# Optimization experiments

Hardware: AMD Instinct MI355X
Metric: run time of the kernel (lower is better)

## Reference

```python
import jax, jax.numpy as jnp
from jax import lax
import numpy as np

ALPHA = 0.82
MAXITER = 10
N1_NODES = 2048
N2_NODES = 2048
K_ATTR = 64
EDGE_P = 0.004  # sparse-ish adjacency density


def setup_inputs() -> dict:
    key = jax.random.key(0)
    k1, k2, k3, k4 = jax.random.split(key, 4)
    A1 = (jax.random.uniform(k1, (N1_NODES, N1_NODES)) < EDGE_P).astype(jnp.float32)
    A1 = jnp.maximum(A1, A1.T)  # undirected 0/1 adjacency
    A2 = (jax.random.uniform(k2, (N2_NODES, N2_NODES)) < EDGE_P).astype(jnp.float32)
    A2 = jnp.maximum(A2, A2.T)
    N1 = jax.random.uniform(k3, (N1_NODES, K_ATTR), dtype=jnp.float32)
    N2 = jax.random.uniform(k4, (N2_NODES, K_ATTR), dtype=jnp.float32)
    # default prior (_get_H with path=None), normalized so sum ~= 1
    H = jnp.full((N2_NODES, N1_NODES), 1.0 / (N1_NODES * N2_NODES), dtype=jnp.float32)
    return {"A1": A1, "A2": A2, "N1": N1, "N2": N2, "H": H}


def _row_l2_normalize(N):
    nrm = jnp.sqrt(jnp.sum(N * N, axis=1, keepdims=True))
    return jnp.where(nrm > 0, N / jnp.where(nrm > 0, nrm, 1.0), 0.0)


def _final_forward(A1, A2, N1, N2, H, alpha=ALPHA, maxiter=MAXITER):
    # No edge attrs: L=1, E1=A1, E2=A2. T = 1/A^2 where A^2>0 (elementwise),
    # E <- E*T, so B = (E*A) = A*T*A.
    def masked_recip_sq(A):
        A2e = A * A
        return jnp.where(A2e > 0, 1.0 / jnp.where(A2e > 0, A2e, 1.0), 0.0)

    B1 = (A1 * masked_recip_sq(A1)) * A1  # (n1, n1)
    B2 = (A2 * masked_recip_sq(A2)) * A2  # (n2, n2)

    N1n = _row_l2_normalize(N1)  # (n1, K)
    N2n = _row_l2_normalize(N2)  # (n2, K)

    # Kronecker vectors laid out as (n1, n2) matrices (C-order == kron order):
    # N[i*n2+j] = sum_k N1[i,k]*N2[j,k]  -> N1n @ N2n.T
    Nm = N1n @ N2n.T  # (n1, n2)
    dm = (B1 @ N1n) @ (B2 @ N2n).T  # (n1, n2)
    D = Nm * dm
    DD = jnp.where(D > 0, lax.rsqrt(jnp.where(D > 0, D, 1.0)), 0.0)  # inf -> 0
    q = DD * Nm  # (n1, n2)

    # h = H.flatten('F') with H (n2,n1): as an (n1,n2) matrix this is H.T
    h = H.T  # (n1, n2)

    def step(s, _):
        # M = (q*s) reshaped (n2,n1) F-order == (q*s).T in our layout.
        # S = B2 @ M @ B1 (n2,n1); S.flatten('F') as (n1,n2) == B1.T @ (q*s) @ B2.T
        S_t = B1.T @ (q * s) @ B2.T  # (n1, n2)
        s_new = (1.0 - alpha) * h + alpha * q * S_t
        return s_new, None

    s, _ = lax.scan(step, h, None, length=maxiter)
    # original: s.reshape((n1, n2)) C-order -> exactly our layout
    return s  # (n1, n2) alignment matrix


def reference(A1, A2, N1, N2, H):
    return _final_forward(A1, A2, N1, N2, H)
```

## Files before the change

### kernel.cpp

```cpp
#include <hip/hip_runtime.h>

#define NMAT 2048
#define KATTR 64
#define CAP 128
#define NITER 10

typedef unsigned short ushort4v __attribute__((ext_vector_type(4)));

__device__ __forceinline__ unsigned short f2bf(float f) {
  unsigned u = __float_as_uint(f);
  return (unsigned short)((u + 0x7fff + ((u >> 16) & 1)) >> 16);
}
__device__ __forceinline__ float bf2f(unsigned short b) {
  return __uint_as_float((unsigned)b << 16);
}
__device__ __forceinline__ float bflo(unsigned v) {
  return __uint_as_float(v << 16);
}
__device__ __forceinline__ float bfhi(unsigned v) {
  return __uint_as_float(v & 0xffff0000u);
}
__device__ __forceinline__ int swz(int c) { return 4 * c + (((c >> 3) & 7) << 2); }

__global__ __launch_bounds__(256) void k_build(
    const float* __restrict__ A, unsigned short* __restrict__ idx,
    unsigned short* __restrict__ idxT, int* __restrict__ cnt) {
  __shared__ int lcnt;
  int r = blockIdx.x;
  if (threadIdx.x == 0) lcnt = 0;
  __syncthreads();
  const float* row = A + (size_t)r * NMAT;
  for (int c = threadIdx.x; c < NMAT; c += 256) {
    if (row[c] != 0.0f) {
      int p = atomicAdd(&lcnt, 1);
      if (p < CAP) {
        idx[r * CAP + p] = (unsigned short)c;
        if (idxT) idxT[(size_t)p * NMAT + r] = (unsigned short)c;
      }
    }
  }
  __syncthreads();
  if (threadIdx.x == 0) cnt[r] = lcnt < CAP ? lcnt : CAP;
}

__global__ __launch_bounds__(256) void k_norm(const float* __restrict__ Nin,
                                              float* __restrict__ Nout) {
  int row = blockIdx.x * 4 + (threadIdx.x >> 6);
  int lane = threadIdx.x & 63;
  float v = Nin[(size_t)row * KATTR + lane];
  float ss = v * v;
#pragma unroll
  for (int o = 32; o > 0; o >>= 1) ss += __shfl_xor(ss, o);
  float nrm = sqrtf(ss);
  Nout[(size_t)row * KATTR + lane] = (nrm > 0.f) ? v / nrm : 0.f;
}

__global__ void k_gatherN(const unsigned short* __restrict__ idx,
                          const int* __restrict__ cnt,
                          const float* __restrict__ Nn,
                          float* __restrict__ C) {
  int i = blockIdx.x;
  int lane = threadIdx.x;
  int nn = cnt[i];
  const unsigned short* ip = idx + i * CAP;
  float acc = 0.f;
  for (int t = 0; t < nn; ++t) {
    int k = ip[t];
    acc += Nn[(size_t)k * KATTR + lane];
  }
  C[(size_t)i * KATTR + lane] = acc;
}

__global__ __launch_bounds__(256) void k_transpose(const float* __restrict__ H,
                                                   float* __restrict__ Ht) {
  __shared__ float tile[64][65];
  int j0 = blockIdx.x * 64;
  int i0 = blockIdx.y * 64;
  int c = threadIdx.x & 63;
  int r0 = threadIdx.x >> 6;
  for (int r = r0; r < 64; r += 4)
    tile[r][c] = H[(size_t)(j0 + r) * NMAT + i0 + c];
  __syncthreads();
  for (int r = r0; r < 64; r += 4)
    Ht[(size_t)(i0 + r) * NMAT + j0 + c] = tile[c][r];
}

__global__ __launch_bounds__(256) void k_q(
    const float* __restrict__ N1n, const float* __restrict__ C1,
    const float* __restrict__ N2n, const float* __restrict__ C2,
    const float* __restrict__ Ht, float* __restrict__ q,
    float* __restrict__ Q2, unsigned short* __restrict__ M,
    unsigned short* __restrict__ M0base) {
  __shared__ float sA[64][68];
  __shared__ float sB[64][68];
  int i0 = blockIdx.y * 64, j0 = blockIdx.x * 64;
  int c = threadIdx.x & 63, r0 = threadIdx.x >> 6;
  int tx = threadIdx.x & 15, ty = threadIdx.x >> 4;
  const float alpha = 0.82f;

  float nmv[4][4] = {};
  float dmv[4][4] = {};

  for (int r = r0; r < 64; r += 4) {
    sA[c][r] = N1n[(size_t)(i0 + r) * KATTR + c];
    sB[c][r] = N2n[(size_t)(j0 + r) * KATTR + c];
  }
  __syncthreads();
#pragma unroll 4
  for (int k = 0; k < 64; ++k) {
    float4 a = *(const float4*)&sA[k][ty * 4];
    float4 b = *(const float4*)&sB[k][tx * 4];
    float av[4] = {a.x, a.y, a.z, a.w};
    float bv[4] = {b.x, b.y, b.z, b.w};
#pragma unroll
    for (int ii = 0; ii < 4; ++ii)
#pragma unroll
      for (int jj = 0; jj < 4; ++jj)
        nmv[ii][jj] = fmaf(av[ii], bv[jj], nmv[ii][jj]);
  }
  __syncthreads();
  for (int r = r0; r < 64; r += 4) {
    sA[c][r] = C1[(size_t)(i0 + r) * KATTR + c];
    sB[c][r] = C2[(size_t)(j0 + r) * KATTR + c];
  }
  __syncthreads();
#pragma unroll 4
  for (int k = 0; k < 64; ++k) {
    float4 a = *(const float4*)&sA[k][ty * 4];
    float4 b = *(const float4*)&sB[k][tx * 4];
    float av[4] = {a.x, a.y, a.z, a.w};
    float bv[4] = {b.x, b.y, b.z, b.w};
#pragma unroll
    for (int ii = 0; ii < 4; ++ii)
#pragma unroll
      for (int jj = 0; jj < 4; ++jj)
        dmv[ii][jj] = fmaf(av[ii], bv[jj], dmv[ii][jj]);
  }

#pragma unroll
  for (int ii = 0; ii < 4; ++ii) {
    int i = i0 + ty * 4 + ii;
    size_t base = (size_t)i * NMAT + j0 + tx * 4;
    float4 hv = *(const float4*)&Ht[base];
    float hvv[4] = {hv.x, hv.y, hv.z, hv.w};
    float qv[4], q2v[4];
    ushort4v mv, m0v;
#pragma unroll
    for (int jj = 0; jj < 4; ++jj) {
      float nmx = nmv[ii][jj];
      float D = nmx * dmv[ii][jj];
      float qq = (D > 0.f) ? nmx * rsqrtf(D) : 0.f;
      qv[jj] = qq;
      q2v[jj] = alpha * qq * qq;
      float m0 = qq * hvv[jj];
      mv[jj] = f2bf(m0);
      m0v[jj] = f2bf((1.0f - alpha) * m0);
    }
    *(float4*)&q[base] = make_float4(qv[0], qv[1], qv[2], qv[3]);
    *(float4*)&Q2[base] = make_float4(q2v[0], q2v[1], q2v[2], q2v[3]);
    *(ushort4v*)&M[base] = mv;
    *(ushort4v*)&M0base[base] = m0v;
  }
}

__global__ __launch_bounds__(1024, 8) void k_iter(
    const unsigned short* __restrict__ idx1, const int* __restrict__ cnt1,
    const unsigned short* __restrict__ idx2T, const int* __restrict__ cnt2,
    const unsigned short* __restrict__ Min, const float* __restrict__ MinF,
    const float* __restrict__ Q2, const unsigned short* __restrict__ M0base,
    const float* __restrict__ q, const float* __restrict__ Ht,
    unsigned short* __restrict__ Mout, float* __restrict__ MoutF,
    float* __restrict__ sout, int in32, int out32, int last) {
  __shared__ float lds[4 * NMAT + 32];
  int i0 = blockIdx.x * 4;
  int tid = threadIdx.x;
  int c0 = tid * 2;

  float acc[4][2];
#pragma unroll
  for (int r = 0; r < 4; ++r) {
    int nn = cnt1[i0 + r];
    const unsigned short* ip = idx1 + (i0 + r) * CAP;
    float a0 = 0.f, a1 = 0.f;
    float b0 = 0.f, b1 = 0.f;
    if (in32) {
      int t = 0;
      for (; t + 4 <= nn; t += 4) {
        uint2 pk = *(const uint2*)(ip + t);
        int k0 = pk.x & 0xffff, k1 = pk.x >> 16;
        int k2 = pk.y & 0xffff, k3 = pk.y >> 16;
        float2 v0 = *(const float2*)(MinF + (size_t)k0 * NMAT + c0);
        float2 v1 = *(const float2*)(MinF + (size_t)k1 * NMAT + c0);
        float2 v2 = *(const float2*)(MinF + (size_t)k2 * NMAT + c0);
        float2 v3 = *(const float2*)(MinF + (size_t)k3 * NMAT + c0);
        a0 += v0.x + v1.x; a1 += v0.y + v1.y;
        b0 += v2.x + v3.x; b1 += v2.y + v3.y;
      }
      for (; t < nn; ++t) {
        float2 v0 = *(const float2*)(MinF + (size_t)ip[t] * NMAT + c0);
        a0 += v0.x; a1 += v0.y;
      }
    } else {
      int t = 0;
      for (; t + 8 <= nn; t += 8) {
        uint4 pk = *(const uint4*)(ip + t);
        int k0 = pk.x & 0xffff, k1 = pk.x >> 16;
        int k2 = pk.y & 0xffff, k3 = pk.y >> 16;
        int k4 = pk.z & 0xffff, k5 = pk.z >> 16;
        int k6 = pk.w & 0xffff, k7 = pk.w >> 16;
        unsigned v0 = *(const unsigned*)(Min + (size_t)k0 * NMAT + c0);
        unsigned v1 = *(const unsigned*)(Min + (size_t)k1 * NMAT + c0);
        unsigned v2 = *(const unsigned*)(Min + (size_t)k2 * NMAT + c0);
        unsigned v3 = *(const unsigned*)(Min + (size_t)k3 * NMAT + c0);
        unsigned v4 = *(const unsigned*)(Min + (size_t)k4 * NMAT + c0);
        unsigned v5 = *(const unsigned*)(Min + (size_t)k5 * NMAT + c0);
        unsigned v6 = *(const unsigned*)(Min + (size_t)k6 * NMAT + c0);
        unsigned v7 = *(const unsigned*)(Min + (size_t)k7 * NMAT + c0);
        a0 += bflo(v0) + bflo(v1) + bflo(v2) + bflo(v3);
        a1 += bfhi(v0) + bfhi(v1) + bfhi(v2) + bfhi(v3);
        b0 += bflo(v4) + bflo(v5) + bflo(v6) + bflo(v7);
        b1 += bfhi(v4) + bfhi(v5) + bfhi(v6) + bfhi(v7);
      }
      for (; t + 4 <= nn; t += 4) {
        uint2 pk = *(const uint2*)(ip + t);
        int k0 = pk.x & 0xffff, k1 = pk.x >> 16;
        int k2 = pk.y & 0xffff, k3 = pk.y >> 16;
        unsigned v0 = *(const unsigned*)(Min + (size_t)k0 * NMAT + c0);
        unsigned v1 = *(const unsigned*)(Min + (size_t)k1 * NMAT + c0);
        unsigned v2 = *(const unsigned*)(Min + (size_t)k2 * NMAT + c0);
        unsigned v3 = *(const unsigned*)(Min + (size_t)k3 * NMAT + c0);
        a0 += bflo(v0) + bflo(v1) + bflo(v2) + bflo(v3);
        a1 += bfhi(v0) + bfhi(v1) + bfhi(v2) + bfhi(v3);
      }
      for (; t < nn; ++t) {
        unsigned v0 = *(const unsigned*)(Min + (size_t)ip[t] * NMAT + c0);
        a0 += bflo(v0); a1 += bfhi(v0);
      }
    }
    acc[r][0] = a0 + b0;
    acc[r][1] = a1 + b1;
  }
  *(float4*)&lds[swz(c0)] =
      make_float4(acc[0][0], acc[1][0], acc[2][0], acc[3][0]);
  *(float4*)&lds[swz(c0 + 1)] =
      make_float4(acc[0][1], acc[1][1], acc[2][1], acc[3][1]);
  __syncthreads();

  const float alpha = 0.82f;
  const float oma = 1.0f - alpha;
#pragma unroll
  for (int jj = 0; jj < 2; ++jj) {
    int j = jj * 1024 + tid;
    int nn = cnt2[j];
    const unsigned short* ip = idx2T + j;
    float s0 = 0.f, s1 = 0.f, s2 = 0.f, s3 = 0.f;
    float u0 = 0.f, u1 = 0.f, u2 = 0.f, u3 = 0.f;
    int t = 0;
    for (; t + 4 <= nn; t += 4) {
      int ka = ip[(size_t)t * NMAT];
      int kb = ip[(size_t)(t + 1) * NMAT];
      int kc = ip[(size_t)(t + 2) * NMAT];
      int kd = ip[(size_t)(t + 3) * NMAT];
      float4 va = *(const float4*)&lds[swz(ka)];
      float4 vb = *(const float4*)&lds[swz(kb)];
      float4 vc = *(const float4*)&lds[swz(kc)];
      float4 vd = *(const float4*)&lds[swz(kd)];
      s0 += va.x + vc.x; s1 += va.y + vc.y;
      s2 += va.z + vc.z; s3 += va.w + vc.w;
      u0 += vb.x + vd.x; u1 += vb.y + vd.y;
      u2 += vb.z + vd.z; u3 += vb.w + vd.w;
    }
    for (; t < nn; ++t) {
      int ka = ip[(size_t)t * NMAT];
      float4 va = *(const float4*)&lds[swz(ka)];
      s0 += va.x; s1 += va.y; s2 += va.z; s3 += va.w;
    }
    float sa[4] = {s0 + u0, s1 + u1, s2 + u2, s3 + u3};
    if (last) {
#pragma unroll
      for (int r = 0; r < 4; ++r) {
        size_t off = (size_t)(i0 + r) * NMAT + j;
        sout[off] = oma * Ht[off] + alpha * q[off] * sa[r];
      }
    } else if (out32) {
#pragma unroll
      for (int r = 0; r < 4; ++r) {
        size_t off = (size_t)(i0 + r) * NMAT + j;
        MoutF[off] = fmaf(Q2[off], sa[r], bf2f(M0base[off]));
      }
    } else {
#pragma unroll
      for (int r = 0; r < 4; ++r) {
        size_t off = (size_t)(i0 + r) * NMAT + j;
        Mout[off] = f2bf(fmaf(Q2[off], sa[r], bf2f(M0base[off])));
      }
    }
  }
}

extern "C" void kernel_launch(void* const* d_in, const int* in_sizes, int n_in,
                              void* d_out, int out_size, void* d_ws,
                              size_t ws_size, hipStream_t stream) {
  const float* A1 = (const float*)d_in[0];
  const float* A2 = (const float*)d_in[1];
  const float* N1 = (const float*)d_in[2];
  const float* N2 = (const float*)d_in[3];
  const float* H = (const float*)d_in[4];
  float* s_out = (float*)d_out;

  char* p = (char*)d_ws;
  auto take = [&](size_t bytes) {
    char* r = p;
    p += (bytes + 255) & ~(size_t)255;
    return r;
  };
  unsigned short* idx1 = (unsigned short*)take((size_t)NMAT * CAP * 2);
  unsigned short* idx2 = (unsigned short*)take((size_t)NMAT * CAP * 2);
  unsigned short* idx2T = (unsigned short*)take((size_t)CAP * NMAT * 2);
  int* cnt1 = (int*)take((size_t)NMAT * 4);
  int* cnt2 = (int*)take((size_t)NMAT * 4);
  float* N1n = (float*)take((size_t)NMAT * KATTR * 4);
  float* N2n = (float*)take((size_t)NMAT * KATTR * 4);
  float* C1 = (float*)take((size_t)NMAT * KATTR * 4);
  float* C2 = (float*)take((size_t)NMAT * KATTR * 4);
  float* Ht = (float*)take((size_t)NMAT * NMAT * 4);
  float* q = (float*)take((size_t)NMAT * NMAT * 4);
  float* Q2 = (float*)take((size_t)NMAT * NMAT * 4);
  unsigned short* Mb0 = (unsigned short*)take((size_t)NMAT * NMAT * 2);
  unsigned short* Mb1 = (unsigned short*)take((size_t)NMAT * NMAT * 2);
  unsigned short* M0b = (unsigned short*)take((size_t)NMAT * NMAT * 2);
  float* Mf = (float*)take((size_t)NMAT * NMAT * 4);
  if ((size_t)(p - (char*)d_ws) > ws_size) return;

  k_build<<<NMAT, 256, 0, stream>>>(A1, idx1, (unsigned short*)nullptr, cnt1);
  k_build<<<NMAT, 256, 0, stream>>>(A2, idx2, idx2T, cnt2);
  k_norm<<<NMAT / 4, 256, 0, stream>>>(N1, N1n);
  k_norm<<<NMAT / 4, 256, 0, stream>>>(N2, N2n);
  k_gatherN<<<NMAT, 64, 0, stream>>>(idx1, cnt1, N1n, C1);
  k_gatherN<<<NMAT, 64, 0, stream>>>(idx2, cnt2, N2n, C2);
  k_transpose<<<dim3(32, 32), 256, 0, stream>>>(H, Ht);
  k_q<<<dim3(32, 32), 256, 0, stream>>>(N1n, C1, N2n, C2, Ht, q, Q2, Mb0,
                                        M0b);
  for (int it = 0; it < NITER; ++it) {
    const unsigned short* Min = (it & 1) ? Mb1 : Mb0;
    unsigned short* Mout = (it & 1) ? Mb0 : Mb1;
    int in32 = (it == NITER - 1) ? 1 : 0;
    int out32 = (it == NITER - 2) ? 1 : 0;
    int last = (it == NITER - 1) ? 1 : 0;
    k_iter<<<NMAT / 4, 1024, 0, stream>>>(idx1, cnt1, idx2T, cnt2, Min, Mf,
                                          Q2, M0b, q, Ht, Mout, Mf, s_out,
                                          in32, out32, last);
  }
}
```

Measured before the change: 460.3 us.

## Restructure sparse iteration kernel: 2 rows per block, wide loads, bf16 LDS, grouped indices

The k_iter kernel now handles 2 output rows per block with 256 threads, each loading 8 contiguous columns per gathered row as 16-byte vectors instead of 4-byte loads. The intermediate row products are stored in LDS as packed bf16 pairs (or float2 on the last step), and the transposed index array is regrouped in blocks of 4 so the second gather fetches 4 indices per load. Epilogue operands are prefetched before the reduction loop. This targets memory-transaction count and index-load overhead, but it adds bf16 rounding of the intermediate in LDS and gives each block fewer rows to reuse the gathered index lists across.

```diff
diff --git a/kernel.cpp b/kernel.cpp
--- a/kernel.cpp
+++ b/kernel.cpp
@@ -20,11 +20,21 @@
 __device__ __forceinline__ float bfhi(unsigned v) {
   return __uint_as_float(v & 0xffff0000u);
 }
-__device__ __forceinline__ int swz(int c) { return 4 * c + (((c >> 3) & 7) << 2); }
+
+__device__ __forceinline__ void addv8(float* a, uint4 v) {
+  a[0] += bflo(v.x); a[1] += bfhi(v.x);
+  a[2] += bflo(v.y); a[3] += bfhi(v.y);
+  a[4] += bflo(v.z); a[5] += bfhi(v.z);
+  a[6] += bflo(v.w); a[7] += bfhi(v.w);
+}
+__device__ __forceinline__ void addf8(float* a, float4 x, float4 y) {
+  a[0] += x.x; a[1] += x.y; a[2] += x.z; a[3] += x.w;
+  a[4] += y.x; a[5] += y.y; a[6] += y.z; a[7] += y.w;
+}
 
 __global__ __launch_bounds__(256) void k_build(
     const float* __restrict__ A, unsigned short* __restrict__ idx,
-    unsigned short* __restrict__ idxT, int* __restrict__ cnt) {
+    unsigned short* __restrict__ idxT4, int* __restrict__ cnt) {
   __shared__ int lcnt;
   int r = blockIdx.x;
   if (threadIdx.x == 0) lcnt = 0;
@@ -35,7 +45,9 @@
       int p = atomicAdd(&lcnt, 1);
       if (p < CAP) {
         idx[r * CAP + p] = (unsigned short)c;
-        if (idxT) idxT[(size_t)p * NMAT + r] = (unsigned short)c;
+        if (idxT4)
+          idxT4[(size_t)(p >> 2) * (NMAT * 4) + r * 4 + (p & 3)] =
+              (unsigned short)c;
       }
     }
   }
@@ -163,137 +175,166 @@
   }
 }
 
-__global__ __launch_bounds__(1024, 8) void k_iter(
+__global__ __launch_bounds__(256, 4) void k_iter(
     const unsigned short* __restrict__ idx1, const int* __restrict__ cnt1,
-    const unsigned short* __restrict__ idx2T, const int* __restrict__ cnt2,
+    const unsigned short* __restrict__ idx2T4, const int* __restrict__ cnt2,
     const unsigned short* __restrict__ Min, const float* __restrict__ MinF,
     const float* __restrict__ Q2, const unsigned short* __restrict__ M0base,
     const float* __restrict__ q, const float* __restrict__ Ht,
     unsigned short* __restrict__ Mout, float* __restrict__ MoutF,
     float* __restrict__ sout, int in32, int out32, int last) {
-  __shared__ float lds[4 * NMAT + 32];
-  int i0 = blockIdx.x * 4;
+  __shared__ float2 ldsF[NMAT + 8];
+  unsigned* ldsU = (unsigned*)ldsF;
+  const int GS = NMAT * 4;
+  int i0 = blockIdx.x * 2;
   int tid = threadIdx.x;
-  int c0 = tid * 2;
-
-  float acc[4][2];
-#pragma unroll
-  for (int r = 0; r < 4; ++r) {
+  int c0 = tid * 8;
+
+  float acc[2][8] = {};
+#pragma unroll
+  for (int r = 0; r < 2; ++r) {
     int nn = cnt1[i0 + r];
     const unsigned short* ip = idx1 + (i0 + r) * CAP;
-    float a0 = 0.f, a1 = 0.f;
-    float b0 = 0.f, b1 = 0.f;
+    float* a = acc[r];
+    int t = 0;
     if (in32) {
-      int t = 0;
+      const float* Mb = MinF;
       for (; t + 4 <= nn; t += 4) {
         uint2 pk = *(const uint2*)(ip + t);
         int k0 = pk.x & 0xffff, k1 = pk.x >> 16;
         int k2 = pk.y & 0xffff, k3 = pk.y >> 16;
-        float2 v0 = *(const float2*)(MinF + (size_t)k0 * NMAT + c0);
-        float2 v1 = *(const float2*)(MinF + (size_t)k1 * NMAT + c0);
-        float2 v2 = *(const float2*)(MinF + (size_t)k2 * NMAT + c0);
-        float2 v3 = *(const float2*)(MinF + (size_t)k3 * NMAT + c0);
-        a0 += v0.x + v1.x; a1 += v0.y + v1.y;
-        b0 += v2.x + v3.x; b1 += v2.y + v3.y;
+        const float* p0 = Mb + (size_t)k0 * NMAT + c0;
+        const float* p1 = Mb + (size_t)k1 * NMAT + c0;
+        const float* p2 = Mb + (size_t)k2 * NMAT + c0;
+        const float* p3 = Mb + (size_t)k3 * NMAT + c0;
+        float4 x0 = *(const float4*)p0, y0 = *(const float4*)(p0 + 4);
+        float4 x1 = *(const float4*)p1, y1 = *(const float4*)(p1 + 4);
+        float4 x2 = *(const float4*)p2, y2 = *(const float4*)(p2 + 4);
+        float4 x3 = *(const float4*)p3, y3 = *(const float4*)(p3 + 4);
+        addf8(a, x0, y0); addf8(a, x1, y1);
+        addf8(a, x2, y2); addf8(a, x3, y3);
       }
       for (; t < nn; ++t) {
-        float2 v0 = *(const float2*)(MinF + (size_t)ip[t] * NMAT + c0);
-        a0 += v0.x; a1 += v0.y;
+        const float* p0 = Mb + (size_t)ip[t] * NMAT + c0;
+        addf8(a, *(const float4*)p0, *(const float4*)(p0 + 4));
       }
     } else {
-      int t = 0;
       for (; t + 8 <= nn; t += 8) {
         uint4 pk = *(const uint4*)(ip + t);
         int k0 = pk.x & 0xffff, k1 = pk.x >> 16;
         int k2 = pk.y & 0xffff, k3 = pk.y >> 16;
         int k4 = pk.z & 0xffff, k5 = pk.z >> 16;
         int k6 = pk.w & 0xffff, k7 = pk.w >> 16;
-        unsigned v0 = *(const unsigned*)(Min + (size_t)k0 * NMAT + c0);
-        unsigned v1 = *(const unsigned*)(Min + (size_t)k1 * NMAT + c0);
-        unsigned v2 = *(const unsigned*)(Min + (size_t)k2 * NMAT + c0);
-        unsigned v3 = *(const unsigned*)(Min + (size_t)k3 * NMAT + c0);
-        unsigned v4 = *(const unsigned*)(Min + (size_t)k4 * NMAT + c0);
-        unsigned v5 = *(const unsigned*)(Min + (size_t)k5 * NMAT + c0);
-        unsigned v6 = *(const unsigned*)(Min + (size_t)k6 * NMAT + c0);
-        unsigned v7 = *(const unsigned*)(Min + (size_t)k7 * NMAT + c0);
-        a0 += bflo(v0) + bflo(v1) + bflo(v2) + bflo(v3);
-        a1 += bfhi(v0) + bfhi(v1) + bfhi(v2) + bfhi(v3);
-        b0 += bflo(v4) + bflo(v5) + bflo(v6) + bflo(v7);
-        b1 += bfhi(v4) + bfhi(v5) + bfhi(v6) + bfhi(v7);
+        uint4 v0 = *(const uint4*)(Min + (size_t)k0 * NMAT + c0);
+        uint4 v1 = *(const uint4*)(Min + (size_t)k1 * NMAT + c0);
+        uint4 v2 = *(const uint4*)(Min + (size_t)k2 * NMAT + c0);
+        uint4 v3 = *(const uint4*)(Min + (size_t)k3 * NMAT + c0);
+        uint4 v4 = *(const uint4*)(Min + (size_t)k4 * NMAT + c0);
+        uint4 v5 = *(const uint4*)(Min + (size_t)k5 * NMAT + c0);
+        uint4 v6 = *(const uint4*)(Min + (size_t)k6 * NMAT + c0);
+        uint4 v7 = *(const uint4*)(Min + (size_t)k7 * NMAT + c0);
+        addv8(a, v0); addv8(a, v1); addv8(a, v2); addv8(a, v3);
+        addv8(a, v4); addv8(a, v5); addv8(a, v6); addv8(a, v7);
       }
       for (; t + 4 <= nn; t += 4) {
         uint2 pk = *(const uint2*)(ip + t);
         int k0 = pk.x & 0xffff, k1 = pk.x >> 16;
         int k2 = pk.y & 0xffff, k3 = pk.y >> 16;
-        unsigned v0 = *(const unsigned*)(Min + (size_t)k0 * NMAT + c0);
-        unsigned v1 = *(const unsigned*)(Min + (size_t)k1 * NMAT + c0);
-        unsigned v2 = *(const unsigned*)(Min + (size_t)k2 * NMAT + c0);
-        unsigned v3 = *(const unsigned*)(Min + (size_t)k3 * NMAT + c0);
-        a0 += bflo(v0) + bflo(v1) + bflo(v2) + bflo(v3);
-        a1 += bfhi(v0) + bfhi(v1) + bfhi(v2) + bfhi(v3);
+        uint4 v0 = *(const uint4*)(Min + (size_t)k0 * NMAT + c0);
+        uint4 v1 = *(const uint4*)(Min + (size_t)k1 * NMAT + c0);
+        uint4 v2 = *(const uint4*)(Min + (size_t)k2 * NMAT + c0);
+        uint4 v3 = *(const uint4*)(Min + (size_t)k3 * NMAT + c0);
+        addv8(a, v0); addv8(a, v1); addv8(a, v2); addv8(a, v3);
       }
       for (; t < nn; ++t) {
-        unsigned v0 = *(const unsigned*)(Min + (size_t)ip[t] * NMAT + c0);
-        a0 += bflo(v0); a1 += bfhi(v0);
-      }
-    }
-    acc[r][0] = a0 + b0;
-    acc[r][1] = a1 + b1;
-  }
-  *(float4*)&lds[swz(c0)] =
-      make_float4(acc[0][0], acc[1][0], acc[2][0], acc[3][0]);
-  *(float4*)&lds[swz(c0 + 1)] =
-      make_float4(acc[0][1], acc[1][1], acc[2][1], acc[3][1]);
+        addv8(a, *(const uint4*)(Min + (size_t)ip[t] * NMAT + c0));
+      }
+    }
+  }
+  if (in32) {
+#pragma unroll
+    for (int cc = 0; cc < 8; ++cc)
+      ldsF[c0 + cc] = make_float2(acc[0][cc], acc[1][cc]);
+  } else {
+    unsigned u[8];
+#pragma unroll
+    for (int cc = 0; cc < 8; ++cc)
+      u[cc] = (unsigned)f2bf(acc[0][cc]) | ((unsigned)f2bf(acc[1][cc]) << 16);
+    *(uint4*)&ldsU[c0] = make_uint4(u[0], u[1], u[2], u[3]);
+    *(uint4*)&ldsU[c0 + 4] = make_uint4(u[4], u[5], u[6], u[7]);
+  }
   __syncthreads();
 
   const float alpha = 0.82f;
   const float oma = 1.0f - alpha;
 #pragma unroll
-  for (int jj = 0; jj < 2; ++jj) {
-    int j = jj * 1024 + tid;
+  for (int jj = 0; jj < 8; ++jj) {
+    int j = jj * 256 + tid;
     int nn = cnt2[j];
-    const unsigned short* ip = idx2T + j;
-    float s0 = 0.f, s1 = 0.f, s2 = 0.f, s3 = 0.f;
-    float u0 = 0.f, u1 = 0.f, u2 = 0.f, u3 = 0.f;
+    const unsigned short* bp = idx2T4 + j * 4;
+    size_t off0 = (size_t)i0 * NMAT + j;
+    size_t off1 = off0 + NMAT;
+    float e0a, e0b, e1a, e1b;
+    if (last) {
+      e0a = Ht[off0]; e0b = q[off0];
+      e1a = Ht[off1]; e1b = q[off1];
+    } else {
+      e0a = Q2[off0]; e0b = bf2f(M0base[off0]);
+      e1a = Q2[off1]; e1b = bf2f(M0base[off1]);
+    }
+    float s0 = 0.f, s1 = 0.f;
     int t = 0;
-    for (; t + 4 <= nn; t += 4) {
-      int ka = ip[(size_t)t * NMAT];
-      int kb = ip[(size_t)(t + 1) * NMAT];
-      int kc = ip[(size_t)(t + 2) * NMAT];
-      int kd = ip[(size_t)(t + 3) * NMAT];
-      float4 va = *(const float4*)&lds[swz(ka)];
-      float4 vb = *(const float4*)&lds[swz(kb)];
-      float4 vc = *(const float4*)&lds[swz(kc)];
-      float4 vd = *(const float4*)&lds[swz(kd)];
-      s0 += va.x + vc.x; s1 += va.y + vc.y;
-      s2 += va.z + vc.z; s3 += va.w + vc.w;
-      u0 += vb.x + vd.x; u1 += vb.y + vd.y;
-      u2 += vb.z + vd.z; u3 += vb.w + vd.w;
-    }
-    for (; t < nn; ++t) {
-      int ka = ip[(size_t)t * NMAT];
-      float4 va = *(const float4*)&lds[swz(ka)];
-      s0 += va.x; s1 += va.y; s2 += va.z; s3 += va.w;
-    }
-    float sa[4] = {s0 + u0, s1 + u1, s2 + u2, s3 + u3};
+    if (in32) {
+      for (; t + 4 <= nn; t += 4) {
+        uint2 ga = *(const uint2*)(bp + (size_t)(t >> 2) * GS);
+        float2 va = ldsF[ga.x & 0xffff];
+        float2 vb = ldsF[ga.x >> 16];
+        float2 vc = ldsF[ga.y & 0xffff];
+        float2 vd = ldsF[ga.y >> 16];
+        s0 += (va.x + vb.x) + (vc.x + vd.x);
+        s1 += (va.y + vb.y) + (vc.y + vd.y);
+      }
+      for (; t < nn; ++t) {
+        int k = bp[(size_t)(t >> 2) * GS + (t & 3)];
+        float2 v = ldsF[k];
+        s0 += v.x; s1 += v.y;
+      }
+    } else {
+      for (; t + 8 <= nn; t += 8) {
+        const unsigned short* gp = bp + (size_t)(t >> 2) * GS;
+        uint2 ga = *(const uint2*)gp;
+        uint2 gb = *(const uint2*)(gp + GS);
+        unsigned w0 = ldsU[ga.x & 0xffff], w1 = ldsU[ga.x >> 16];
+        unsigned w2 = ldsU[ga.y & 0xffff], w3 = ldsU[ga.y >> 16];
+        unsigned w4 = ldsU[gb.x & 0xffff], w5 = ldsU[gb.x >> 16];
+        unsigned w6 = ldsU[gb.y & 0xffff], w7 = ldsU[gb.y >> 16];
+        s0 += (bflo(w0) + bflo(w1)) + (bflo(w2) + bflo(w3)) +
+              (bflo(w4) + bflo(w5)) + (bflo(w6) + bflo(w7));
+        s1 += (bfhi(w0) + bfhi(w1)) + (bfhi(w2) + bfhi(w3)) +
+              (bfhi(w4) + bfhi(w5)) + (bfhi(w6) + bfhi(w7));
+      }
+      for (; t + 4 <= nn; t += 4) {
+        uint2 ga = *(const uint2*)(bp + (size_t)(t >> 2) * GS);
+        unsigned w0 = ldsU[ga.x & 0xffff], w1 = ldsU[ga.x >> 16];
+        unsigned w2 = ldsU[ga.y & 0xffff], w3 = ldsU[ga.y >> 16];
+        s0 += (bflo(w0) + bflo(w1)) + (bflo(w2) + bflo(w3));
+        s1 += (bfhi(w0) + bfhi(w1)) + (bfhi(w2) + bfhi(w3));
+      }
+      for (; t < nn; ++t) {
+        int k = bp[(size_t)(t >> 2) * GS + (t & 3)];
+        unsigned w = ldsU[k];
+        s0 += bflo(w); s1 += bfhi(w);
+      }
+    }
     if (last) {
-#pragma unroll
-      for (int r = 0; r < 4; ++r) {
-        size_t off = (size_t)(i0 + r) * NMAT + j;
-        sout[off] = oma * Ht[off] + alpha * q[off] * sa[r];
-      }
+      sout[off0] = oma * e0a + alpha * e0b * s0;
+      sout[off1] = oma * e1a + alpha * e1b * s1;
     } else if (out32) {
-#pragma unroll
-      for (int r = 0; r < 4; ++r) {
-        size_t off = (size_t)(i0 + r) * NMAT + j;
-        MoutF[off] = fmaf(Q2[off], sa[r], bf2f(M0base[off]));
-      }
+      MoutF[off0] = fmaf(e0a, s0, e0b);
+      MoutF[off1] = fmaf(e1a, s1, e1b);
     } else {
-#pragma unroll
-      for (int r = 0; r < 4; ++r) {
-        size_t off = (size_t)(i0 + r) * NMAT + j;
-        Mout[off] = f2bf(fmaf(Q2[off], sa[r], bf2f(M0base[off])));
-      }
+      Mout[off0] = f2bf(fmaf(e0a, s0, e0b));
+      Mout[off1] = f2bf(fmaf(e1a, s1, e1b));
     }
   }
 }
@@ -316,7 +357,7 @@
   };
   unsigned short* idx1 = (unsigned short*)take((size_t)NMAT * CAP * 2);
   unsigned short* idx2 = (unsigned short*)take((size_t)NMAT * CAP * 2);
-  unsigned short* idx2T = (unsigned short*)take((size_t)CAP * NMAT * 2);
+  unsigned short* idx2T4 = (unsigned short*)take((size_t)CAP * NMAT * 2);
   int* cnt1 = (int*)take((size_t)NMAT * 4);
   int* cnt2 = (int*)take((size_t)NMAT * 4);
   float* N1n = (float*)take((size_t)NMAT * KATTR * 4);
@@ -333,7 +374,7 @@
   if ((size_t)(p - (char*)d_ws) > ws_size) return;
 
   k_build<<<NMAT, 256, 0, stream>>>(A1, idx1, (unsigned short*)nullptr, cnt1);
-  k_build<<<NMAT, 256, 0, stream>>>(A2, idx2, idx2T, cnt2);
+  k_build<<<NMAT, 256, 0, stream>>>(A2, idx2, idx2T4, cnt2);
   k_norm<<<NMAT / 4, 256, 0, stream>>>(N1, N1n);
   k_norm<<<NMAT / 4, 256, 0, stream>>>(N2, N2n);
   k_gatherN<<<NMAT, 64, 0, stream>>>(idx1, cnt1, N1n, C1);
@@ -347,8 +388,8 @@
     int in32 = (it == NITER - 1) ? 1 : 0;
     int out32 = (it == NITER - 2) ? 1 : 0;
     int last = (it == NITER - 1) ? 1 : 0;
-    k_iter<<<NMAT / 4, 1024, 0, stream>>>(idx1, cnt1, idx2T, cnt2, Min, Mf,
-                                          Q2, M0b, q, Ht, Mout, Mf, s_out,
-                                          in32, out32, last);
-  }
-}
+    k_iter<<<NMAT / 2, 256, 0, stream>>>(idx1, cnt1, idx2T4, cnt2, Min, Mf,
+                                         Q2, M0b, q, Ht, Mout, Mf, s_out,
+                                         in32, out32, last);
+  }
+}
```

Result: slower. 554.5 us (+20.5%).

## Pad sparse index lists with sentinels and pack coefficients into one bf16 word

Applied to the files above, without the earlier changes.

Pads each adjacency row's neighbour list with sentinel indices that point at a zero row (in global memory) or a zero LDS slot. The gather loops can then issue a fixed unrolled batch of 16–32 loads with no count-dependent tails, and remainder loops only run for high-degree rows. The transposed index array is re-laid-out in groups of 4 so each thread fetches 4 indices per uint2 load. Q2 and M0base are packed as two bf16 halves of one 32-bit word and loaded before the gather, which cuts per-iteration traffic. The cost is wasted loads on low-degree rows and Q2 dropping from fp32 to bf16 precision.

```diff
diff --git a/kernel.cpp b/kernel.cpp
--- a/kernel.cpp
+++ b/kernel.cpp
@@ -4,6 +4,8 @@
 #define KATTR 64
 #define CAP 128
 #define NITER 10
+#define SENT_A 2048
+#define SENT_B 2057
 
 typedef unsigned short ushort4v __attribute__((ext_vector_type(4)));
 
@@ -24,7 +26,7 @@
 
 __global__ __launch_bounds__(256) void k_build(
     const float* __restrict__ A, unsigned short* __restrict__ idx,
-    unsigned short* __restrict__ idxT, int* __restrict__ cnt) {
+    unsigned short* __restrict__ idxT4, int* __restrict__ cnt) {
   __shared__ int lcnt;
   int r = blockIdx.x;
   if (threadIdx.x == 0) lcnt = 0;
@@ -35,12 +37,21 @@
       int p = atomicAdd(&lcnt, 1);
       if (p < CAP) {
         idx[r * CAP + p] = (unsigned short)c;
-        if (idxT) idxT[(size_t)p * NMAT + r] = (unsigned short)c;
-      }
-    }
-  }
-  __syncthreads();
-  if (threadIdx.x == 0) cnt[r] = lcnt < CAP ? lcnt : CAP;
+        if (idxT4)
+          idxT4[(size_t)(p >> 2) * (NMAT * 4) + r * 4 + (p & 3)] =
+              (unsigned short)c;
+      }
+    }
+  }
+  __syncthreads();
+  int n = lcnt < CAP ? lcnt : CAP;
+  for (int p = n + threadIdx.x; p < CAP; p += 256) {
+    idx[r * CAP + p] = (unsigned short)SENT_A;
+    if (idxT4)
+      idxT4[(size_t)(p >> 2) * (NMAT * 4) + r * 4 + (p & 3)] =
+          (unsigned short)SENT_B;
+  }
+  if (threadIdx.x == 0) cnt[r] = n;
 }
 
 __global__ __launch_bounds__(256) void k_norm(const float* __restrict__ Nin,
@@ -85,12 +96,22 @@
     Ht[(size_t)(i0 + r) * NMAT + j0 + c] = tile[c][r];
 }
 
+__global__ __launch_bounds__(1024) void k_zrow(unsigned short* __restrict__ Mb0,
+                                               unsigned short* __restrict__ Mb1,
+                                               float* __restrict__ Mf) {
+  size_t Z = (size_t)NMAT * NMAT;
+  for (int o = threadIdx.x; o < NMAT; o += 1024) {
+    Mb0[Z + o] = 0;
+    Mb1[Z + o] = 0;
+    Mf[Z + o] = 0.f;
+  }
+}
+
 __global__ __launch_bounds__(256) void k_q(
     const float* __restrict__ N1n, const float* __restrict__ C1,
     const float* __restrict__ N2n, const float* __restrict__ C2,
     const float* __restrict__ Ht, float* __restrict__ q,
-    float* __restrict__ Q2, unsigned short* __restrict__ M,
-    unsigned short* __restrict__ M0base) {
+    unsigned* __restrict__ QM, unsigned short* __restrict__ M) {
   __shared__ float sA[64][68];
   __shared__ float sB[64][68];
   int i0 = blockIdx.y * 64, j0 = blockIdx.x * 64;
@@ -143,102 +164,138 @@
     size_t base = (size_t)i * NMAT + j0 + tx * 4;
     float4 hv = *(const float4*)&Ht[base];
     float hvv[4] = {hv.x, hv.y, hv.z, hv.w};
-    float qv[4], q2v[4];
-    ushort4v mv, m0v;
+    float qv[4];
+    unsigned qmv[4];
+    ushort4v mv;
 #pragma unroll
     for (int jj = 0; jj < 4; ++jj) {
       float nmx = nmv[ii][jj];
       float D = nmx * dmv[ii][jj];
       float qq = (D > 0.f) ? nmx * rsqrtf(D) : 0.f;
       qv[jj] = qq;
-      q2v[jj] = alpha * qq * qq;
       float m0 = qq * hvv[jj];
       mv[jj] = f2bf(m0);
-      m0v[jj] = f2bf((1.0f - alpha) * m0);
+      qmv[jj] = (unsigned)f2bf(alpha * qq * qq) |
+                ((unsigned)f2bf((1.0f - alpha) * m0) << 16);
     }
     *(float4*)&q[base] = make_float4(qv[0], qv[1], qv[2], qv[3]);
-    *(float4*)&Q2[base] = make_float4(q2v[0], q2v[1], q2v[2], q2v[3]);
+    *(uint4*)&QM[base] = make_uint4(qmv[0], qmv[1], qmv[2], qmv[3]);
     *(ushort4v*)&M[base] = mv;
-    *(ushort4v*)&M0base[base] = m0v;
   }
 }
 
 __global__ __launch_bounds__(1024, 8) void k_iter(
     const unsigned short* __restrict__ idx1, const int* __restrict__ cnt1,
-    const unsigned short* __restrict__ idx2T, const int* __restrict__ cnt2,
+    const unsigned short* __restrict__ idx2T4, const int* __restrict__ cnt2,
     const unsigned short* __restrict__ Min, const float* __restrict__ MinF,
-    const float* __restrict__ Q2, const unsigned short* __restrict__ M0base,
-    const float* __restrict__ q, const float* __restrict__ Ht,
-    unsigned short* __restrict__ Mout, float* __restrict__ MoutF,
-    float* __restrict__ sout, int in32, int out32, int last) {
-  __shared__ float lds[4 * NMAT + 32];
+    const unsigned* __restrict__ QM, const float* __restrict__ q,
+    const float* __restrict__ Ht, unsigned short* __restrict__ Mout,
+    float* __restrict__ MoutF, float* __restrict__ sout, int in32, int out32,
+    int last) {
+  __shared__ float lds[4 * NMAT + 64];
+  const int GS = NMAT * 4;
   int i0 = blockIdx.x * 4;
   int tid = threadIdx.x;
   int c0 = tid * 2;
 
+  if (tid == 0) *(float4*)&lds[swz(SENT_B)] = make_float4(0.f, 0.f, 0.f, 0.f);
+
   float acc[4][2];
 #pragma unroll
   for (int r = 0; r < 4; ++r) {
     int nn = cnt1[i0 + r];
     const unsigned short* ip = idx1 + (i0 + r) * CAP;
+    uint4 pA = *(const uint4*)(ip);
+    uint4 pB = *(const uint4*)(ip + 8);
+    uint4 pC = *(const uint4*)(ip + 16);
+    uint4 pD = *(const uint4*)(ip + 24);
     float a0 = 0.f, a1 = 0.f;
-    float b0 = 0.f, b1 = 0.f;
     if (in32) {
-      int t = 0;
-      for (; t + 4 <= nn; t += 4) {
-        uint2 pk = *(const uint2*)(ip + t);
-        int k0 = pk.x & 0xffff, k1 = pk.x >> 16;
-        int k2 = pk.y & 0xffff, k3 = pk.y >> 16;
-        float2 v0 = *(const float2*)(MinF + (size_t)k0 * NMAT + c0);
-        float2 v1 = *(const float2*)(MinF + (size_t)k1 * NMAT + c0);
-        float2 v2 = *(const float2*)(MinF + (size_t)k2 * NMAT + c0);
-        float2 v3 = *(const float2*)(MinF + (size_t)k3 * NMAT + c0);
-        a0 += v0.x + v1.x; a1 += v0.y + v1.y;
-        b0 += v2.x + v3.x; b1 += v2.y + v3.y;
-      }
-      for (; t < nn; ++t) {
-        float2 v0 = *(const float2*)(MinF + (size_t)ip[t] * NMAT + c0);
-        a0 += v0.x; a1 += v0.y;
+      const float* Bf = MinF + c0;
+      auto g8f = [&](uint4 pk, float2* w) {
+        w[0] = *(const float2*)(Bf + (size_t)(pk.x & 0xffff) * NMAT);
+        w[1] = *(const float2*)(Bf + (size_t)(pk.x >> 16) * NMAT);
+        w[2] = *(const float2*)(Bf + (size_t)(pk.y & 0xffff) * NMAT);
+        w[3] = *(const float2*)(Bf + (size_t)(pk.y >> 16) * NMAT);
+        w[4] = *(const float2*)(Bf + (size_t)(pk.z & 0xffff) * NMAT);
+        w[5] = *(const float2*)(Bf + (size_t)(pk.z >> 16) * NMAT);
+        w[6] = *(const float2*)(Bf + (size_t)(pk.w & 0xffff) * NMAT);
+        w[7] = *(const float2*)(Bf + (size_t)(pk.w >> 16) * NMAT);
+      };
+      float2 w[16];
+      g8f(pA, w);
+      g8f(pB, w + 8);
+#pragma unroll
+      for (int e = 0; e < 16; ++e) {
+        a0 += w[e].x;
+        a1 += w[e].y;
+      }
+      if (nn > 16) {
+        float2 w2[16];
+        g8f(pC, w2);
+        g8f(pD, w2 + 8);
+#pragma unroll
+        for (int e = 0; e < 16; ++e) {
+          a0 += w2[e].x;
+          a1 += w2[e].y;
+        }
+      }
+      for (int t = 32; t < nn; t += 8) {
+        uint4 pk = *(const uint4*)(ip + t);
+        float2 w3[8];
+        g8f(pk, w3);
+#pragma unroll
+        for (int e = 0; e < 8; ++e) {
+          a0 += w3[e].x;
+          a1 += w3[e].y;
+        }
       }
     } else {
-      int t = 0;
-      for (; t + 8 <= nn; t += 8) {
+      const unsigned short* Bb = Min + c0;
+      auto g8 = [&](uint4 pk, unsigned* w) {
+        w[0] = *(const unsigned*)(Bb + (size_t)(pk.x & 0xffff) * NMAT);
+        w[1] = *(const unsigned*)(Bb + (size_t)(pk.x >> 16) * NMAT);
+        w[2] = *(const unsigned*)(Bb + (size_t)(pk.y & 0xffff) * NMAT);
+        w[3] = *(const unsigned*)(Bb + (size_t)(pk.y >> 16) * NMAT);
+        w[4] = *(const unsigned*)(Bb + (size_t)(pk.z & 0xffff) * NMAT);
+        w[5] = *(const unsigned*)(Bb + (size_t)(pk.z >> 16) * NMAT);
+        w[6] = *(const unsigned*)(Bb + (size_t)(pk.w & 0xffff) * NMAT);
+        w[7] = *(const unsigned*)(Bb + (size_t)(pk.w >> 16) * NMAT);
+      };
+      unsigned w[16];
+      g8(pA, w);
+      g8(pB, w + 8);
+      bool more = nn > 16;
+      unsigned w2[16];
+      if (more) {
+        g8(pC, w2);
+        g8(pD, w2 + 8);
+      }
+#pragma unroll
+      for (int e = 0; e < 16; ++e) {
+        a0 += bflo(w[e]);
+        a1 += bfhi(w[e]);
+      }
+      if (more) {
+#pragma unroll
+        for (int e = 0; e < 16; ++e) {
+          a0 += bflo(w2[e]);
+          a1 += bfhi(w2[e]);
+        }
+      }
+      for (int t = 32; t < nn; t += 8) {
         uint4 pk = *(const uint4*)(ip + t);
-        int k0 = pk.x & 0xffff, k1 = pk.x >> 16;
-        int k2 = pk.y & 0xffff, k3 = pk.y >> 16;
-        int k4 = pk.z & 0xffff, k5 = pk.z >> 16;
-        int k6 = pk.w & 0xffff, k7 = pk.w >> 16;
-        unsigned v0 = *(const unsigned*)(Min + (size_t)k0 * NMAT + c0);
-        unsigned v1 = *(const unsigned*)(Min + (size_t)k1 * NMAT + c0);
-        unsigned v2 = *(const unsigned*)(Min + (size_t)k2 * NMAT + c0);
-        unsigned v3 = *(const unsigned*)(Min + (size_t)k3 * NMAT + c0);
-        unsigned v4 = *(const unsigned*)(Min + (size_t)k4 * NMAT + c0);
-        unsigned v5 = *(const unsigned*)(Min + (size_t)k5 * NMAT + c0);
-        unsigned v6 = *(const unsigned*)(Min + (size_t)k6 * NMAT + c0);
-        unsigned v7 = *(const unsigned*)(Min + (size_t)k7 * NMAT + c0);
-        a0 += bflo(v0) + bflo(v1) + bflo(v2) + bflo(v3);
-        a1 += bfhi(v0) + bfhi(v1) + bfhi(v2) + bfhi(v3);
-        b0 += bflo(v4) + bflo(v5) + bflo(v6) + bflo(v7);
-        b1 += bfhi(v4) + bfhi(v5) + bfhi(v6) + bfhi(v7);
-      }
-      for (; t + 4 <= nn; t += 4) {
-        uint2 pk = *(const uint2*)(ip + t);
-        int k0 = pk.x & 0xffff, k1 = pk.x >> 16;
-        int k2 = pk.y & 0xffff, k3 = pk.y >> 16;
-        unsigned v0 = *(const unsigned*)(Min + (size_t)k0 * NMAT + c0);
-        unsigned v1 = *(const unsigned*)(Min + (size_t)k1 * NMAT + c0);
-        unsigned v2 = *(const unsigned*)(Min + (size_t)k2 * NMAT + c0);
-        unsigned v3 = *(const unsigned*)(Min + (size_t)k3 * NMAT + c0);
-        a0 += bflo(v0) + bflo(v1) + bflo(v2) + bflo(v3);
-        a1 += bfhi(v0) + bfhi(v1) + bfhi(v2) + bfhi(v3);
-      }
-      for (; t < nn; ++t) {
-        unsigned v0 = *(const unsigned*)(Min + (size_t)ip[t] * NMAT + c0);
-        a0 += bflo(v0); a1 += bfhi(v0);
-      }
-    }
-    acc[r][0] = a0 + b0;
-    acc[r][1] = a1 + b1;
+        unsigned w3[8];
+        g8(pk, w3);
+#pragma unroll
+        for (int e = 0; e < 8; ++e) {
+          a0 += bflo(w3[e]);
+          a1 += bfhi(w3[e]);
+        }
+      }
+    }
+    acc[r][0] = a0;
+    acc[r][1] = a1;
   }
   *(float4*)&lds[swz(c0)] =
       make_float4(acc[0][0], acc[1][0], acc[2][0], acc[3][0]);
@@ -252,48 +309,94 @@
   for (int jj = 0; jj < 2; ++jj) {
     int j = jj * 1024 + tid;
     int nn = cnt2[j];
-    const unsigned short* ip = idx2T + j;
+    const unsigned short* bp = idx2T4 + j * 4;
+    size_t off0 = (size_t)i0 * NMAT + j;
+    unsigned wq0 = 0, wq1 = 0, wq2 = 0, wq3 = 0;
+    if (!last) {
+      wq0 = QM[off0];
+      wq1 = QM[off0 + NMAT];
+      wq2 = QM[off0 + 2 * NMAT];
+      wq3 = QM[off0 + 3 * NMAT];
+    }
+    uint2 g0 = *(const uint2*)(bp);
+    uint2 g1 = *(const uint2*)(bp + GS);
+    uint2 g2 = *(const uint2*)(bp + 2 * GS);
+    uint2 g3 = *(const uint2*)(bp + 3 * GS);
     float s0 = 0.f, s1 = 0.f, s2 = 0.f, s3 = 0.f;
     float u0 = 0.f, u1 = 0.f, u2 = 0.f, u3 = 0.f;
-    int t = 0;
-    for (; t + 4 <= nn; t += 4) {
-      int ka = ip[(size_t)t * NMAT];
-      int kb = ip[(size_t)(t + 1) * NMAT];
-      int kc = ip[(size_t)(t + 2) * NMAT];
-      int kd = ip[(size_t)(t + 3) * NMAT];
-      float4 va = *(const float4*)&lds[swz(ka)];
-      float4 vb = *(const float4*)&lds[swz(kb)];
-      float4 vc = *(const float4*)&lds[swz(kc)];
-      float4 vd = *(const float4*)&lds[swz(kd)];
-      s0 += va.x + vc.x; s1 += va.y + vc.y;
-      s2 += va.z + vc.z; s3 += va.w + vc.w;
-      u0 += vb.x + vd.x; u1 += vb.y + vd.y;
-      u2 += vb.z + vd.z; u3 += vb.w + vd.w;
-    }
-    for (; t < nn; ++t) {
-      int ka = ip[(size_t)t * NMAT];
-      float4 va = *(const float4*)&lds[swz(ka)];
-      s0 += va.x; s1 += va.y; s2 += va.z; s3 += va.w;
+    {
+      float4 va = *(const float4*)&lds[swz(g0.x & 0xffff)];
+      float4 vb = *(const float4*)&lds[swz(g0.x >> 16)];
+      float4 vc = *(const float4*)&lds[swz(g0.y & 0xffff)];
+      float4 vd = *(const float4*)&lds[swz(g0.y >> 16)];
+      float4 ve = *(const float4*)&lds[swz(g1.x & 0xffff)];
+      float4 vf = *(const float4*)&lds[swz(g1.x >> 16)];
+      float4 vg = *(const float4*)&lds[swz(g1.y & 0xffff)];
+      float4 vh = *(const float4*)&lds[swz(g1.y >> 16)];
+      s0 += (va.x + vb.x) + (vc.x + vd.x);
+      s1 += (va.y + vb.y) + (vc.y + vd.y);
+      s2 += (va.z + vb.z) + (vc.z + vd.z);
+      s3 += (va.w + vb.w) + (vc.w + vd.w);
+      u0 += (ve.x + vf.x) + (vg.x + vh.x);
+      u1 += (ve.y + vf.y) + (vg.y + vh.y);
+      u2 += (ve.z + vf.z) + (vg.z + vh.z);
+      u3 += (ve.w + vf.w) + (vg.w + vh.w);
+    }
+    {
+      float4 va = *(const float4*)&lds[swz(g2.x & 0xffff)];
+      float4 vb = *(const float4*)&lds[swz(g2.x >> 16)];
+      float4 vc = *(const float4*)&lds[swz(g2.y & 0xffff)];
+      float4 vd = *(const float4*)&lds[swz(g2.y >> 16)];
+      float4 ve = *(const float4*)&lds[swz(g3.x & 0xffff)];
+      float4 vf = *(const float4*)&lds[swz(g3.x >> 16)];
+      float4 vg = *(const float4*)&lds[swz(g3.y & 0xffff)];
+      float4 vh = *(const float4*)&lds[swz(g3.y >> 16)];
+      s0 += (va.x + vb.x) + (vc.x + vd.x);
+      s1 += (va.y + vb.y) + (vc.y + vd.y);
+      s2 += (va.z + vb.z) + (vc.z + vd.z);
+      s3 += (va.w + vb.w) + (vc.w + vd.w);
+      u0 += (ve.x + vf.x) + (vg.x + vh.x);
+      u1 += (ve.y + vf.y) + (vg.y + vh.y);
+      u2 += (ve.z + vf.z) + (vg.z + vh.z);
+      u3 += (ve.w + vf.w) + (vg.w + vh.w);
+    }
+    for (int t = 16; t < nn; t += 8) {
+      uint2 ga = *(const uint2*)(bp + (size_t)(t >> 2) * GS);
+      uint2 gb = *(const uint2*)(bp + (size_t)((t >> 2) + 1) * GS);
+      float4 va = *(const float4*)&lds[swz(ga.x & 0xffff)];
+      float4 vb = *(const float4*)&lds[swz(ga.x >> 16)];
+      float4 vc = *(const float4*)&lds[swz(ga.y & 0xffff)];
+      float4 vd = *(const float4*)&lds[swz(ga.y >> 16)];
+      float4 ve = *(const float4*)&lds[swz(gb.x & 0xffff)];
+      float4 vf = *(const float4*)&lds[swz(gb.x >> 16)];
+      float4 vg = *(const float4*)&lds[swz(gb.y & 0xffff)];
+      float4 vh = *(const float4*)&lds[swz(gb.y >> 16)];
+      s0 += (va.x + vb.x) + (vc.x + vd.x);
+      s1 += (va.y + vb.y) + (vc.y + vd.y);
+      s2 += (va.z + vb.z) + (vc.z + vd.z);
+      s3 += (va.w + vb.w) + (vc.w + vd.w);
+      u0 += (ve.x + vf.x) + (vg.x + vh.x);
+      u1 += (ve.y + vf.y) + (vg.y + vh.y);
+      u2 += (ve.z + vf.z) + (vg.z + vh.z);
+      u3 += (ve.w + vf.w) + (vg.w + vh.w);
     }
     float sa[4] = {s0 + u0, s1 + u1, s2 + u2, s3 + u3};
     if (last) {
 #pragma unroll
       for (int r = 0; r < 4; ++r) {
-        size_t off = (size_t)(i0 + r) * NMAT + j;
+        size_t off = off0 + (size_t)r * NMAT;
         sout[off] = oma * Ht[off] + alpha * q[off] * sa[r];
       }
     } else if (out32) {
-#pragma unroll
-      for (int r = 0; r < 4; ++r) {
-        size_t off = (size_t)(i0 + r) * NMAT + j;
-        MoutF[off] = fmaf(Q2[off], sa[r], bf2f(M0base[off]));
-      }
+      MoutF[off0] = fmaf(bflo(wq0), sa[0], bfhi(wq0));
+      MoutF[off0 + NMAT] = fmaf(bflo(wq1), sa[1], bfhi(wq1));
+      MoutF[off0 + 2 * NMAT] = fmaf(bflo(wq2), sa[2], bfhi(wq2));
+      MoutF[off0 + 3 * NMAT] = fmaf(bflo(wq3), sa[3], bfhi(wq3));
     } else {
-#pragma unroll
-      for (int r = 0; r < 4; ++r) {
-        size_t off = (size_t)(i0 + r) * NMAT + j;
-        Mout[off] = f2bf(fmaf(Q2[off], sa[r], bf2f(M0base[off])));
-      }
+      Mout[off0] = f2bf(fmaf(bflo(wq0), sa[0], bfhi(wq0)));
+      Mout[off0 + NMAT] = f2bf(fmaf(bflo(wq1), sa[1], bfhi(wq1)));
+      Mout[off0 + 2 * NMAT] = f2bf(fmaf(bflo(wq2), sa[2], bfhi(wq2)));
+      Mout[off0 + 3 * NMAT] = f2bf(fmaf(bflo(wq3), sa[3], bfhi(wq3)));
     }
   }
 }
@@ -316,7 +419,7 @@
   };
   unsigned short* idx1 = (unsigned short*)take((size_t)NMAT * CAP * 2);
   unsigned short* idx2 = (unsigned short*)take((size_t)NMAT * CAP * 2);
-  unsigned short* idx2T = (unsigned short*)take((size_t)CAP * NMAT * 2);
+  unsigned short* idx2T4 = (unsigned short*)take((size_t)CAP * NMAT * 2);
   int* cnt1 = (int*)take((size_t)NMAT * 4);
   int* cnt2 = (int*)take((size_t)NMAT * 4);
   float* N1n = (float*)take((size_t)NMAT * KATTR * 4);
@@ -325,30 +428,29 @@
   float* C2 = (float*)take((size_t)NMAT * KATTR * 4);
   float* Ht = (float*)take((size_t)NMAT * NMAT * 4);
   float* q = (float*)take((size_t)NMAT * NMAT * 4);
-  float* Q2 = (float*)take((size_t)NMAT * NMAT * 4);
-  unsigned short* Mb0 = (unsigned short*)take((size_t)NMAT * NMAT * 2);
-  unsigned short* Mb1 = (unsigned short*)take((size_t)NMAT * NMAT * 2);
-  unsigned short* M0b = (unsigned short*)take((size_t)NMAT * NMAT * 2);
-  float* Mf = (float*)take((size_t)NMAT * NMAT * 4);
+  unsigned* QM = (unsigned*)take((size_t)NMAT * NMAT * 4);
+  unsigned short* Mb0 = (unsigned short*)take((size_t)(NMAT + 1) * NMAT * 2);
+  unsigned short* Mb1 = (unsigned short*)take((size_t)(NMAT + 1) * NMAT * 2);
+  float* Mf = (float*)take((size_t)(NMAT + 1) * NMAT * 4);
   if ((size_t)(p - (char*)d_ws) > ws_size) return;
 
   k_build<<<NMAT, 256, 0, stream>>>(A1, idx1, (unsigned short*)nullptr, cnt1);
-  k_build<<<NMAT, 256, 0, stream>>>(A2, idx2, idx2T, cnt2);
+  k_build<<<NMAT, 256, 0, stream>>>(A2, idx2, idx2T4, cnt2);
   k_norm<<<NMAT / 4, 256, 0, stream>>>(N1, N1n);
   k_norm<<<NMAT / 4, 256, 0, stream>>>(N2, N2n);
   k_gatherN<<<NMAT, 64, 0, stream>>>(idx1, cnt1, N1n, C1);
   k_gatherN<<<NMAT, 64, 0, stream>>>(idx2, cnt2, N2n, C2);
   k_transpose<<<dim3(32, 32), 256, 0, stream>>>(H, Ht);
-  k_q<<<dim3(32, 32), 256, 0, stream>>>(N1n, C1, N2n, C2, Ht, q, Q2, Mb0,
-                                        M0b);
+  k_q<<<dim3(32, 32), 256, 0, stream>>>(N1n, C1, N2n, C2, Ht, q, QM, Mb0);
+  k_zrow<<<1, 1024, 0, stream>>>(Mb0, Mb1, Mf);
   for (int it = 0; it < NITER; ++it) {
     const unsigned short* Min = (it & 1) ? Mb1 : Mb0;
     unsigned short* Mout = (it & 1) ? Mb0 : Mb1;
     int in32 = (it == NITER - 1) ? 1 : 0;
     int out32 = (it == NITER - 2) ? 1 : 0;
     int last = (it == NITER - 1) ? 1 : 0;
-    k_iter<<<NMAT / 4, 1024, 0, stream>>>(idx1, cnt1, idx2T, cnt2, Min, Mf,
-                                          Q2, M0b, q, Ht, Mout, Mf, s_out,
-                                          in32, out32, last);
-  }
-}
+    k_iter<<<NMAT / 4, 1024, 0, stream>>>(idx1, cnt1, idx2T4, cnt2, Min, Mf,
+                                          QM, q, Ht, Mout, Mf, s_out, in32,
+                                          out32, last);
+  }
+}
```

After: 426.1 us. 7.4% less time.
